# Kernel tuning notes

Hardware: AMD Instinct MI355X
Metric: run time of the kernel (lower is better)

## Reference

```python
import jax, jax.numpy as jnp
import numpy as np

T, C_IN, H_IN, W_IN = 15, 2, 1020, 1020
CONV1_T_PASS, CONV2_T_PASS, CONV3_T = 5.0, 50.0, 40.0
K3, R3 = 2, 5

def _pad2(x, p=2):
    return jnp.pad(x, ((0, 0), (0, 0), (p, p), (p, p)))

def _conv(x, w):
    return jax.lax.conv_general_dilated(x, w, (1, 1), 'VALID', dimension_numbers=('NCHW', 'OIHW', 'NCHW'))

def _fire(pot, thr):
    # SpykeTorch sf.fire: spikes where potential >= threshold, thresholded potentials
    spk = (pot >= thr).astype(pot.dtype)
    return spk, pot * spk

def _pool(x):
    # F.max_pool2d(kernel=2, stride=2, padding=1)
    return jax.lax.reduce_window(x, -jnp.inf, jax.lax.max, (1, 1, 2, 2), (1, 1, 2, 2), ((0, 0), (0, 0), (1, 1), (1, 1)))

def _get_k_winners(pot, spk, k, r):
    # SpykeTorch k-winners-take-all: earliest-spike priority, then sequential
    # argmax with whole-feature-map and spatial-radius (r) inhibition (NMS-like)
    T_, C, H, W = pot.shape
    maximum = (T_ - spk.sum(0)).astype(pot.dtype)  # (C,H,W): fewer active timesteps -> earlier spike gets higher priority
    trunc = spk * pot
    v = trunc.max(0) * maximum                      # (C,H,W)
    total = (trunc + spk * v[None]).sum(0)          # (C,H,W)
    cs, ys, xs = jnp.arange(C), jnp.arange(H), jnp.arange(W)

    def step(i, state):
        total, winners = state
        flat = total.reshape(-1)
        idx = jnp.argmax(flat).astype(jnp.int32)
        val = flat[idx]
        c = idx // (H * W)
        rem = idx % (H * W)
        y = rem // W
        x = rem % W
        valid = val > 0
        win = jnp.where(valid, jnp.stack([c, y, x]), jnp.full((3,), -1, jnp.int32))
        winners = winners.at[i].set(win)
        feat_keep = (cs != c)[:, None, None]        # suppress whole winning feature map
        sp_keep = ((jnp.abs(ys - y) > r)[:, None] | (jnp.abs(xs - x) > r)[None, :])[None]  # columnar inhibition
        total = jnp.where(valid, total * (feat_keep | sp_keep), total)
        return total, winners

    winners0 = jnp.full((k, 3), -1, jnp.int32)
    _, winners = jax.lax.fori_loop(0, k, step, (total, winners0))
    return winners

def setup_inputs():
    key = jax.random.key(0)
    k_in, k2, k3 = jax.random.split(key, 3)
    # binary cumulative spike-wave input (SpykeTorch temporal coding)
    raw = jax.random.uniform(k_in, (T, C_IN, H_IN, W_IN)) < 0.1
    inp = jnp.clip(jnp.cumsum(raw.astype(jnp.float32), axis=0), 0.0, 1.0)
    # fixed conv1 weights from __init__ (4 oriented 5x5 filters), repeated over 2 in-channels
    d = np.full((4, 5, 5), 0.25, np.float32)
    d[0, 2, :] = 0.75
    d[1, :, :2] = 0.75
    m2 = np.array([[1,0,0,0,0],[0,1,1,0,0],[0,1,1,1,0],[0,0,1,1,0],[0,0,0,0,1]], np.float32)
    d[2] = 0.25 + 0.5 * m2
    m3 = np.array([[0,0,0,0,1],[0,0,1,1,0],[0,1,1,1,0],[0,1,1,0,0],[1,0,0,0,0]], np.float32)
    d[3] = 0.25 + 0.5 * m3
    w1 = jnp.asarray(np.repeat(d[:, None], 2, axis=1))        # (4,2,5,5)
    w2 = 0.8 + 0.05 * jax.random.normal(k2, (8, 4, 15, 15))   # snn.Convolution(4,8,15,0.8,0.05)
    w3 = 0.8 + 0.05 * jax.random.normal(k3, (2, 8, 7, 7))     # snn.Convolution(8,2,7,0.8,0.05)
    return {"input": inp, "w1": w1, "w2": w2, "w3": w3, "max_layer": 3}

def reference(input, w1, w2, w3, max_layer):
    assert max_layer == 3
    pot = _conv(_pad2(input), w1)                 # (15,4,1020,1020)
    spk, pot = _fire(pot, CONV1_T_PASS)
    pot = _conv(_pad2(_pool(spk)), w2)            # (15,8,501,501)
    spk, pot = _fire(pot, CONV2_T_PASS)
    pot = _conv(_pad2(_pool(spk)), w3)            # (15,2,249,249)
    spk, pot = _fire(pot, CONV3_T)                # fire at conv3_t is idempotent on thresholded pot
    winners = _get_k_winners(pot, spk, K3, R3)
    return spk, pot, winners
```

## Files before the change

### kernel.cpp

```cpp
#include <hip/hip_runtime.h>

#define HW_IN 1020
#define P1 511
#define H2 501
#define P2 251
#define H3 249
#define OUT_SPK 0
#define OUT_POT (15*2*249*249)
#define OUT_WIN (2*15*2*249*249)

__global__ __launch_bounds__(256) void k_tau_in(const float* __restrict__ in,
                                                unsigned char* __restrict__ tau) {
    const int n = 2 * HW_IN * HW_IN;
    int i = blockIdx.x * 256 + threadIdx.x;
    if (i >= n) return;
    float s = 0.f;
#pragma unroll
    for (int t = 0; t < 15; ++t) s += in[(size_t)t * n + i];
    tau[i] = (unsigned char)(15 - (int)(s + 0.5f));
}

__global__ __launch_bounds__(256) void k_conv1_pool(const unsigned char* __restrict__ tin,
                                                    const float* __restrict__ w1,
                                                    unsigned char* __restrict__ t1p) {
    const int c4 = blockIdx.z;
    const int X0 = blockIdx.x * 16, Y0 = blockIdx.y * 16;
    __shared__ unsigned char sm[2][36][36];
    __shared__ float sw[2][5][5];
    const int tid = threadIdx.y * 16 + threadIdx.x;
    if (tid < 50) {
        int cin = tid / 25, r = tid % 25;
        sw[cin][r / 5][r % 5] = w1[(c4 * 2 + cin) * 25 + r];
    }
    for (int s = tid; s < 2 * 36 * 36; s += 256) {
        int cin = s / (36 * 36), rem = s % (36 * 36), rr = rem / 36, cc = rem % 36;
        int y = 2 * Y0 - 3 + rr, x = 2 * X0 - 3 + cc;
        unsigned char v = 15;
        if (y >= 0 && y < HW_IN && x >= 0 && x < HW_IN)
            v = tin[(cin * HW_IN + y) * HW_IN + x];
        sm[cin][rr][cc] = v;
    }
    __syncthreads();
    const int py = Y0 + threadIdx.y, px = X0 + threadIdx.x;
    if (py >= P1 || px >= P1) return;

    int rg[2][6][6];
#pragma unroll
    for (int cin = 0; cin < 2; ++cin)
#pragma unroll
        for (int rr = 0; rr < 6; ++rr)
#pragma unroll
            for (int cc = 0; cc < 6; ++cc)
                rg[cin][rr][cc] = sm[cin][2 * threadIdx.y + rr][2 * threadIdx.x + cc];
    float wr[2][5][5];
#pragma unroll
    for (int cin = 0; cin < 2; ++cin)
#pragma unroll
        for (int ky = 0; ky < 5; ++ky)
#pragma unroll
            for (int kx = 0; kx < 5; ++kx) wr[cin][ky][kx] = sw[cin][ky][kx];

    const bool va0 = (py >= 1);
    const bool va1 = (py <= 509);
    const bool vb0 = (px >= 1);
    const bool vb1 = (px <= 509);

    int lo = 0, hi = 15;
    while (lo < hi) {
        const int mid = (lo + hi) >> 1;
        bool any = false;
#pragma unroll
        for (int a = 0; a < 2; ++a) {
#pragma unroll
            for (int b = 0; b < 2; ++b) {
                const bool valid = (a ? va1 : va0) && (b ? vb1 : vb0);
                float s = 0.f;
#pragma unroll
                for (int cin = 0; cin < 2; ++cin)
#pragma unroll
                    for (int ky = 0; ky < 5; ++ky)
#pragma unroll
                        for (int kx = 0; kx < 5; ++kx)
                            s += (rg[cin][a + ky][b + kx] <= mid) ? wr[cin][ky][kx] : 0.f;
                any = any || (valid && s >= 5.0f);
            }
        }
        if (any) hi = mid; else lo = mid + 1;
    }
    t1p[(c4 * P1 + py) * P1 + px] = (unsigned char)lo;
}

__global__ __launch_bounds__(128) void k_conv2_pool(const unsigned char* __restrict__ t1p,
                                                    const float* __restrict__ w2,
                                                    unsigned char* __restrict__ t2p) {
    const int oc = blockIdx.z;
    const int X0 = blockIdx.x * 32, Y0 = blockIdx.y * 16;
    __shared__ unsigned char stau[4][47][80];
    __shared__ unsigned char sdel[4][47][80];
    __shared__ float sw[4][15][16];
    __shared__ int undone;
    const int tx = threadIdx.x, ty = threadIdx.y;
    const int tid = ty * 8 + tx;

    for (int s = tid; s < 4 * 225; s += 128) {
        int c = s / 225, r = s % 225;
        sw[c][r / 15][r % 15] = w2[(oc * 4 + c) * 225 + r];
    }
    for (int s = tid; s < 4 * 47 * 80; s += 128) {
        int c = s / (47 * 80), rem = s % (47 * 80), rr = rem / 80, cc = rem % 80;
        int y = 2 * Y0 - 3 + rr, x = 2 * X0 - 3 + cc;
        unsigned char v = 15;
        if (y >= 0 && y < P1 && x >= 0 && x < P1)
            v = t1p[(c * P1 + y) * P1 + x];
        stau[c][rr][cc] = v;
    }

    const int py = Y0 + ty;
    const int pxb = X0 + tx * 4;
    float acc[4][4];
#pragma unroll
    for (int j = 0; j < 4; ++j) { acc[j][0] = acc[j][1] = acc[j][2] = acc[j][3] = 0.f; }
    int taup[4] = {15, 15, 15, 15};
    bool vj[4], vb0[4];
#pragma unroll
    for (int j = 0; j < 4; ++j) {
        vj[j] = (py < P2) && (pxb + j < P2);
        vb0[j] = (pxb + j >= 1);
    }
    const bool va0 = (py >= 1);

    __syncthreads();
    for (int t = 0; t < 15; ++t) {
        if (tid == 0) undone = 0;
        __syncthreads();
        bool act = false;
#pragma unroll
        for (int j = 0; j < 4; ++j) act |= (vj[j] && taup[j] == 15);
        if (act) undone = 1;
        __syncthreads();
        if (undone == 0) break;
        {
            const unsigned int rep = 0x01010101u * (unsigned)t;
            const unsigned int* src = (const unsigned int*)&stau[0][0][0];
            unsigned int* dst = (unsigned int*)&sdel[0][0][0];
            for (int s = tid; s < (4 * 47 * 80) / 4; s += 128) {
                unsigned int x = src[s] ^ rep;
                unsigned int y = (x | 0x80808080u) - 0x01010101u;
                dst[s] = (~y & 0x80808080u) >> 7;
            }
        }
        __syncthreads();
        if (act) {
#pragma clang loop unroll(disable)
            for (int c = 0; c < 4; ++c) {
#pragma clang loop unroll(disable)
                for (int u = 0; u < 16; ++u) {
                    const int rr = 2 * ty + u;
                    const unsigned int* rp = (const unsigned int*)&sdel[c][rr][0] + 2 * tx;
                    unsigned int d[6];
#pragma unroll
                    for (int q = 0; q < 6; ++q) d[q] = rp[q];
                    float f[24];
#pragma unroll
                    for (int q = 0; q < 6; ++q) {
                        f[4 * q + 0] = (float)(d[q] & 0xFFu);
                        f[4 * q + 1] = (float)((d[q] >> 8) & 0xFFu);
                        f[4 * q + 2] = (float)((d[q] >> 16) & 0xFFu);
                        f[4 * q + 3] = (float)(d[q] >> 24);
                    }
#pragma unroll
                    for (int a = 0; a < 2; ++a) {
                        const int ky = u - a;
                        if (ky < 0 || ky >= 15) continue;
                        const float* wrow = &sw[c][ky][0];
#pragma unroll
                        for (int kx = 0; kx < 15; ++kx) {
                            const float wv = wrow[kx];
#pragma unroll
                            for (int j = 0; j < 4; ++j) {
                                acc[j][a * 2 + 0] += wv * f[2 * j + 0 + kx];
                                acc[j][a * 2 + 1] += wv * f[2 * j + 1 + kx];
                            }
                        }
                    }
                }
            }
#pragma unroll
            for (int j = 0; j < 4; ++j) {
                if (vj[j] && taup[j] == 15) {
                    bool fired = false;
                    fired |= (va0 && vb0[j] && acc[j][0] >= 50.f);
                    fired |= (va0 &&           acc[j][1] >= 50.f);
                    fired |= (       vb0[j] && acc[j][2] >= 50.f);
                    fired |= (                 acc[j][3] >= 50.f);
                    if (fired) taup[j] = t;
                }
            }
        }
        __syncthreads();
    }
#pragma unroll
    for (int j = 0; j < 4; ++j)
        if (vj[j]) t2p[(oc * P2 + py) * P2 + pxb + j] = (unsigned char)taup[j];
}

__global__ __launch_bounds__(256) void k_conv3_out(const unsigned char* __restrict__ t2p,
                                                   const float* __restrict__ w3,
                                                   float* __restrict__ out,
                                                   float* __restrict__ total) {
    const int oc = blockIdx.z;
    const int X0 = blockIdx.x * 16, Y0 = blockIdx.y * 16;
    __shared__ unsigned char st[8][22][24];
    __shared__ float sw[8][7][7];
    const int tid = threadIdx.y * 16 + threadIdx.x;
    for (int i = tid; i < 8 * 49; i += 256) {
        int c = i / 49, r = i % 49;
        sw[c][r / 7][r % 7] = w3[(oc * 8 + c) * 49 + r];
    }
    for (int i = tid; i < 8 * 22 * 24; i += 256) {
        int c = i / (22 * 24), rem = i % (22 * 24), rr = rem / 24, cc = rem % 24;
        int y = Y0 - 2 + rr, x = X0 - 2 + cc;
        unsigned char v = 15;
        if (y >= 0 && y < P2 && x >= 0 && x < P2)
            v = t2p[(c * P2 + y) * P2 + x];
        st[c][rr][cc] = v;
    }
    __syncthreads();
    const int oy = Y0 + threadIdx.y, ox = X0 + threadIdx.x;
    if (oy >= H3 || ox >= H3) return;
    float s[15];
#pragma unroll
    for (int t = 0; t < 15; ++t) s[t] = 0.f;
    for (int c = 0; c < 8; ++c) {
#pragma unroll
        for (int ky = 0; ky < 7; ++ky) {
#pragma unroll
            for (int kx = 0; kx < 7; ++kx) {
                const int tv = st[c][threadIdx.y + ky][threadIdx.x + kx];
                const float wv = sw[c][ky][kx];
#pragma unroll
                for (int t = 0; t < 15; ++t) s[t] += (tv <= t) ? wv : 0.f;
            }
        }
    }
    int n = 0;
    float S = 0.f, M = 0.f;
    const int base = (oc * H3 + oy) * H3 + ox;
#pragma unroll
    for (int t = 0; t < 15; ++t) {
        const bool sp = (s[t] >= 40.f);
        const float pv = sp ? s[t] : 0.f;
        n += sp ? 1 : 0;
        S += pv;
        M = fmaxf(M, pv);
        out[OUT_SPK + t * (2 * H3 * H3) + base] = sp ? 1.f : 0.f;
        out[OUT_POT + t * (2 * H3 * H3) + base] = pv;
    }
    total[base] = S + (float)n * (M * (float)(15 - n));
}

__device__ __forceinline__ unsigned long long pack_wi(float v, int i) {
    return ((unsigned long long)__float_as_uint(v) << 32) |
           (unsigned long long)(0xFFFFFFFFu - (unsigned)i);
}

__global__ __launch_bounds__(256) void k_win_pass(const float* __restrict__ total,
                                                  unsigned long long* __restrict__ state,
                                                  int pass) {
    const int N = 2 * H3 * H3;
    int c0 = -1, y0 = 0, x0 = 0;
    bool inh = false;
    if (pass == 1) {
        const unsigned long long s0 = state[0];
        const float v0 = __uint_as_float((unsigned)(s0 >> 32));
        if (v0 > 0.f) {
            const unsigned i0 = 0xFFFFFFFFu - (unsigned)(s0 & 0xFFFFFFFFu);
            c0 = (int)(i0 / (H3 * H3));
            const int rem = (int)(i0 % (H3 * H3));
            y0 = rem / H3; x0 = rem % H3;
            inh = true;
        }
    }
    unsigned long long best = 0;
    for (int i = blockIdx.x * 256 + threadIdx.x; i < N; i += gridDim.x * 256) {
        if (inh) {
            const int ci = i / (H3 * H3), rem = i % (H3 * H3);
            const int yi = rem / H3, xi = rem % H3;
            if (ci == c0 && yi >= y0 - 5 && yi <= y0 + 5 && xi >= x0 - 5 && xi <= x0 + 5)
                continue;
        }
        const unsigned long long p = pack_wi(total[i], i);
        if (p > best) best = p;
    }
#pragma unroll
    for (int off = 32; off; off >>= 1) {
        const unsigned long long o = __shfl_down(best, off, 64);
        if (o > best) best = o;
    }
    if ((threadIdx.x & 63) == 0)
        atomicMax(&state[pass], best);
}

__global__ void k_win_finish(const unsigned long long* __restrict__ state,
                             float* __restrict__ out) {
    const int k = threadIdx.x;
    if (k >= 2) return;
    const unsigned long long s = state[k];
    const float v = __uint_as_float((unsigned)(s >> 32));
    const bool valid = (v > 0.f);
    const unsigned i = 0xFFFFFFFFu - (unsigned)(s & 0xFFFFFFFFu);
    const int c = (int)(i / (H3 * H3));
    const int rem = (int)(i % (H3 * H3));
    const int y = rem / H3, x = rem % H3;
    out[OUT_WIN + k * 3 + 0] = valid ? (float)c : -1.f;
    out[OUT_WIN + k * 3 + 1] = valid ? (float)y : -1.f;
    out[OUT_WIN + k * 3 + 2] = valid ? (float)x : -1.f;
}

extern "C" void kernel_launch(void* const* d_in, const int* in_sizes, int n_in,
                              void* d_out, int out_size, void* d_ws, size_t ws_size,
                              hipStream_t stream) {
    (void)in_sizes; (void)n_in; (void)out_size; (void)ws_size;
    const float* inp = (const float*)d_in[0];
    const float* w1 = (const float*)d_in[1];
    const float* w2 = (const float*)d_in[2];
    const float* w3 = (const float*)d_in[3];
    float* out = (float*)d_out;
    char* ws = (char*)d_ws;

    unsigned char* tau_in = (unsigned char*)ws;
    unsigned char* t1p = (unsigned char*)(ws + 2 * HW_IN * HW_IN);
    unsigned char* t2p = t1p + 4 * P1 * P1;
    size_t tot_off = (size_t)(2 * HW_IN * HW_IN) + 4 * P1 * P1 + 8 * P2 * P2;
    tot_off = (tot_off + 15) & ~(size_t)15;
    float* total = (float*)(ws + tot_off);
    unsigned long long* win_state =
        (unsigned long long*)(ws + tot_off + (size_t)2 * H3 * H3 * 4);

    hipMemsetAsync(win_state, 0, 2 * sizeof(unsigned long long), stream);
    k_tau_in<<<dim3((2 * HW_IN * HW_IN + 255) / 256), dim3(256), 0, stream>>>(inp, tau_in);
    k_conv1_pool<<<dim3(32, 32, 4), dim3(16, 16), 0, stream>>>(tau_in, w1, t1p);
    k_conv2_pool<<<dim3(8, 16, 8), dim3(8, 16), 0, stream>>>(t1p, w2, t2p);
    k_conv3_out<<<dim3(16, 16, 2), dim3(16, 16), 0, stream>>>(t2p, w3, out, total);
    k_win_pass<<<dim3(128), dim3(256), 0, stream>>>(total, win_state, 0);
    k_win_pass<<<dim3(128), dim3(256), 0, stream>>>(total, win_state, 1);
    k_win_finish<<<dim3(1), dim3(64), 0, stream>>>(win_state, out);
}
```

Before: 465.3 us.

## Shrink conv2 blocks to one wavefront, skip zero rows, fuse first winner pass

Result: slower. 546.2 us (+17.4%).

```diff
diff --git a/kernel.cpp b/kernel.cpp
--- a/kernel.cpp
+++ b/kernel.cpp
@@ -12,12 +12,21 @@
 __global__ __launch_bounds__(256) void k_tau_in(const float* __restrict__ in,
                                                 unsigned char* __restrict__ tau) {
     const int n = 2 * HW_IN * HW_IN;
+    const int n4 = n / 4;
     int i = blockIdx.x * 256 + threadIdx.x;
-    if (i >= n) return;
-    float s = 0.f;
-#pragma unroll
-    for (int t = 0; t < 15; ++t) s += in[(size_t)t * n + i];
-    tau[i] = (unsigned char)(15 - (int)(s + 0.5f));
+    if (i >= n4) return;
+    float4 s = make_float4(0.f, 0.f, 0.f, 0.f);
+#pragma unroll
+    for (int t = 0; t < 15; ++t) {
+        const float4 v = ((const float4*)(in + (size_t)t * n))[i];
+        s.x += v.x; s.y += v.y; s.z += v.z; s.w += v.w;
+    }
+    uchar4 r;
+    r.x = (unsigned char)(15 - (int)(s.x + 0.5f));
+    r.y = (unsigned char)(15 - (int)(s.y + 0.5f));
+    r.z = (unsigned char)(15 - (int)(s.z + 0.5f));
+    r.w = (unsigned char)(15 - (int)(s.w + 0.5f));
+    ((uchar4*)tau)[i] = r;
 }
 
 __global__ __launch_bounds__(256) void k_conv1_pool(const unsigned char* __restrict__ tin,
@@ -90,24 +99,23 @@
     t1p[(c4 * P1 + py) * P1 + px] = (unsigned char)lo;
 }
 
-__global__ __launch_bounds__(128) void k_conv2_pool(const unsigned char* __restrict__ t1p,
-                                                    const float* __restrict__ w2,
-                                                    unsigned char* __restrict__ t2p) {
+__global__ __launch_bounds__(64) void k_conv2_pool(const unsigned char* __restrict__ t1p,
+                                                   const float* __restrict__ w2,
+                                                   unsigned char* __restrict__ t2p) {
     const int oc = blockIdx.z;
-    const int X0 = blockIdx.x * 32, Y0 = blockIdx.y * 16;
-    __shared__ unsigned char stau[4][47][80];
-    __shared__ unsigned char sdel[4][47][80];
+    const int X0 = blockIdx.x * 16, Y0 = blockIdx.y * 16;
+    __shared__ unsigned char stau[4][47][48];
+    __shared__ unsigned char sdel[4][47][48];
     __shared__ float sw[4][15][16];
-    __shared__ int undone;
     const int tx = threadIdx.x, ty = threadIdx.y;
-    const int tid = ty * 8 + tx;
-
-    for (int s = tid; s < 4 * 225; s += 128) {
+    const int tid = ty * 4 + tx;
+
+    for (int s = tid; s < 4 * 225; s += 64) {
         int c = s / 225, r = s % 225;
         sw[c][r / 15][r % 15] = w2[(oc * 4 + c) * 225 + r];
     }
-    for (int s = tid; s < 4 * 47 * 80; s += 128) {
-        int c = s / (47 * 80), rem = s % (47 * 80), rr = rem / 80, cc = rem % 80;
+    for (int s = tid; s < 4 * 47 * 48; s += 64) {
+        int c = s / (47 * 48), rem = s % (47 * 48), rr = rem / 48, cc = rem % 48;
         int y = 2 * Y0 - 3 + rr, x = 2 * X0 - 3 + cc;
         unsigned char v = 15;
         if (y >= 0 && y < P1 && x >= 0 && x < P1)
@@ -131,19 +139,16 @@
 
     __syncthreads();
     for (int t = 0; t < 15; ++t) {
-        if (tid == 0) undone = 0;
+        bool act = false;
+#pragma unroll
+        for (int j = 0; j < 4; ++j) act |= (vj[j] && taup[j] == 15);
+        if (__ballot(act) == 0ull) break;
         __syncthreads();
-        bool act = false;
-#pragma unroll
-        for (int j = 0; j < 4; ++j) act |= (vj[j] && taup[j] == 15);
-        if (act) undone = 1;
-        __syncthreads();
-        if (undone == 0) break;
         {
             const unsigned int rep = 0x01010101u * (unsigned)t;
             const unsigned int* src = (const unsigned int*)&stau[0][0][0];
             unsigned int* dst = (unsigned int*)&sdel[0][0][0];
-            for (int s = tid; s < (4 * 47 * 80) / 4; s += 128) {
+            for (int s = tid; s < (4 * 47 * 48) / 4; s += 64) {
                 unsigned int x = src[s] ^ rep;
                 unsigned int y = (x | 0x80808080u) - 0x01010101u;
                 dst[s] = (~y & 0x80808080u) >> 7;
@@ -160,6 +165,8 @@
                     unsigned int d[6];
 #pragma unroll
                     for (int q = 0; q < 6; ++q) d[q] = rp[q];
+                    const unsigned int dz = d[0] | d[1] | d[2] | d[3] | d[4] | d[5];
+                    if (dz == 0u) continue;
                     float f[24];
 #pragma unroll
                     for (int q = 0; q < 6; ++q) {
@@ -197,21 +204,27 @@
                 }
             }
         }
-        __syncthreads();
     }
 #pragma unroll
     for (int j = 0; j < 4; ++j)
         if (vj[j]) t2p[(oc * P2 + py) * P2 + pxb + j] = (unsigned char)taup[j];
+}
+
+__device__ __forceinline__ unsigned long long pack_wi(float v, int i) {
+    return ((unsigned long long)__float_as_uint(v) << 32) |
+           (unsigned long long)(0xFFFFFFFFu - (unsigned)i);
 }
 
 __global__ __launch_bounds__(256) void k_conv3_out(const unsigned char* __restrict__ t2p,
                                                    const float* __restrict__ w3,
                                                    float* __restrict__ out,
-                                                   float* __restrict__ total) {
+                                                   float* __restrict__ total,
+                                                   unsigned long long* __restrict__ state) {
     const int oc = blockIdx.z;
     const int X0 = blockIdx.x * 16, Y0 = blockIdx.y * 16;
     __shared__ unsigned char st[8][22][24];
     __shared__ float sw[8][7][7];
+    __shared__ unsigned long long wred[4];
     const int tid = threadIdx.y * 16 + threadIdx.x;
     for (int i = tid; i < 8 * 49; i += 256) {
         int c = i / 49, r = i % 49;
@@ -227,50 +240,63 @@
     }
     __syncthreads();
     const int oy = Y0 + threadIdx.y, ox = X0 + threadIdx.x;
-    if (oy >= H3 || ox >= H3) return;
-    float s[15];
-#pragma unroll
-    for (int t = 0; t < 15; ++t) s[t] = 0.f;
-    for (int c = 0; c < 8; ++c) {
-#pragma unroll
-        for (int ky = 0; ky < 7; ++ky) {
-#pragma unroll
-            for (int kx = 0; kx < 7; ++kx) {
-                const int tv = st[c][threadIdx.y + ky][threadIdx.x + kx];
-                const float wv = sw[c][ky][kx];
-#pragma unroll
-                for (int t = 0; t < 15; ++t) s[t] += (tv <= t) ? wv : 0.f;
-            }
-        }
-    }
-    int n = 0;
-    float S = 0.f, M = 0.f;
-    const int base = (oc * H3 + oy) * H3 + ox;
-#pragma unroll
-    for (int t = 0; t < 15; ++t) {
-        const bool sp = (s[t] >= 40.f);
-        const float pv = sp ? s[t] : 0.f;
-        n += sp ? 1 : 0;
-        S += pv;
-        M = fmaxf(M, pv);
-        out[OUT_SPK + t * (2 * H3 * H3) + base] = sp ? 1.f : 0.f;
-        out[OUT_POT + t * (2 * H3 * H3) + base] = pv;
-    }
-    total[base] = S + (float)n * (M * (float)(15 - n));
-}
-
-__device__ __forceinline__ unsigned long long pack_wi(float v, int i) {
-    return ((unsigned long long)__float_as_uint(v) << 32) |
-           (unsigned long long)(0xFFFFFFFFu - (unsigned)i);
-}
-
-__global__ __launch_bounds__(256) void k_win_pass(const float* __restrict__ total,
-                                                  unsigned long long* __restrict__ state,
-                                                  int pass) {
+    const bool valid = (oy < H3) && (ox < H3);
+    unsigned long long p = 0;
+    if (valid) {
+        float s[15];
+#pragma unroll
+        for (int t = 0; t < 15; ++t) s[t] = 0.f;
+        for (int c = 0; c < 8; ++c) {
+#pragma unroll
+            for (int ky = 0; ky < 7; ++ky) {
+#pragma unroll
+                for (int kx = 0; kx < 7; ++kx) {
+                    const int tv = st[c][threadIdx.y + ky][threadIdx.x + kx];
+                    const float wv = sw[c][ky][kx];
+#pragma unroll
+                    for (int t = 0; t < 15; ++t) s[t] += (tv <= t) ? wv : 0.f;
+                }
+            }
+        }
+        int n = 0;
+        float S = 0.f, M = 0.f;
+        const int base = (oc * H3 + oy) * H3 + ox;
+#pragma unroll
+        for (int t = 0; t < 15; ++t) {
+            const bool sp = (s[t] >= 40.f);
+            const float pv = sp ? s[t] : 0.f;
+            n += sp ? 1 : 0;
+            S += pv;
+            M = fmaxf(M, pv);
+            out[OUT_SPK + t * (2 * H3 * H3) + base] = sp ? 1.f : 0.f;
+            out[OUT_POT + t * (2 * H3 * H3) + base] = pv;
+        }
+        const float tot = S + (float)n * (M * (float)(15 - n));
+        total[base] = tot;
+        p = pack_wi(tot, base);
+    }
+#pragma unroll
+    for (int off = 32; off; off >>= 1) {
+        const unsigned long long o = __shfl_down(p, off, 64);
+        if (o > p) p = o;
+    }
+    if ((tid & 63) == 0) wred[tid >> 6] = p;
+    __syncthreads();
+    if (tid == 0) {
+        unsigned long long m = wred[0];
+        if (wred[1] > m) m = wred[1];
+        if (wred[2] > m) m = wred[2];
+        if (wred[3] > m) m = wred[3];
+        atomicMax(&state[0], m);
+    }
+}
+
+__global__ __launch_bounds__(256) void k_win_pass1(const float* __restrict__ total,
+                                                   unsigned long long* __restrict__ state) {
     const int N = 2 * H3 * H3;
     int c0 = -1, y0 = 0, x0 = 0;
     bool inh = false;
-    if (pass == 1) {
+    {
         const unsigned long long s0 = state[0];
         const float v0 = __uint_as_float((unsigned)(s0 >> 32));
         if (v0 > 0.f) {
@@ -298,7 +324,7 @@
         if (o > best) best = o;
     }
     if ((threadIdx.x & 63) == 0)
-        atomicMax(&state[pass], best);
+        atomicMax(&state[1], best);
 }
 
 __global__ void k_win_finish(const unsigned long long* __restrict__ state,
@@ -338,11 +364,10 @@
         (unsigned long long*)(ws + tot_off + (size_t)2 * H3 * H3 * 4);
 
     hipMemsetAsync(win_state, 0, 2 * sizeof(unsigned long long), stream);
-    k_tau_in<<<dim3((2 * HW_IN * HW_IN + 255) / 256), dim3(256), 0, stream>>>(inp, tau_in);
+    k_tau_in<<<dim3((2 * HW_IN * HW_IN / 4 + 255) / 256), dim3(256), 0, stream>>>(inp, tau_in);
     k_conv1_pool<<<dim3(32, 32, 4), dim3(16, 16), 0, stream>>>(tau_in, w1, t1p);
-    k_conv2_pool<<<dim3(8, 16, 8), dim3(8, 16), 0, stream>>>(t1p, w2, t2p);
-    k_conv3_out<<<dim3(16, 16, 2), dim3(16, 16), 0, stream>>>(t2p, w3, out, total);
-    k_win_pass<<<dim3(128), dim3(256), 0, stream>>>(total, win_state, 0);
-    k_win_pass<<<dim3(128), dim3(256), 0, stream>>>(total, win_state, 1);
+    k_conv2_pool<<<dim3(16, 16, 8), dim3(4, 16), 0, stream>>>(t1p, w2, t2p);
+    k_conv3_out<<<dim3(16, 16, 2), dim3(16, 16), 0, stream>>>(t2p, w3, out, total, win_state);
+    k_win_pass1<<<dim3(128), dim3(256), 0, stream>>>(total, win_state);
     k_win_finish<<<dim3(1), dim3(64), 0, stream>>>(win_state, out);
 }
```
